# Kernel optimization log

Hardware: AMD Instinct MI355X
Metric: run time of the kernel (lower is better)

## Reference

```python
import jax, jax.numpy as jnp
import numpy as np
from jax import lax

HEADS = 8
LN_EPS = 1e-5


def setup_inputs() -> dict:
    key = jax.random.key(0)
    k = jax.random.split(key, 8)
    B, C, H, W, r = 4, 64, 64, 64, 4
    T = H * W
    x = jax.random.normal(k[0], (B, C, H, W), dtype=jnp.float32)
    conv_w = jax.random.normal(k[1], (C, C, r, r), dtype=jnp.float32) * 0.02  # OIHW
    conv_b = jnp.zeros((C,), dtype=jnp.float32)
    ln_g = jnp.ones((C,), dtype=jnp.float32)
    ln_b = jnp.zeros((C,), dtype=jnp.float32)
    Wqkv = jax.random.normal(k[2], (C, 3 * C), dtype=jnp.float32) * 0.02  # to_qvk (no bias)
    W0 = jax.random.normal(k[3], (C, C), dtype=jnp.float32) * 0.02  # output proj (no bias)
    E = jax.random.normal(k[4], (T, T // 4), dtype=jnp.float32)  # Linformer proj (randn in torch fwd)
    return {"x": x, "conv_w": conv_w, "conv_b": conv_b, "ln_g": ln_g,
            "ln_b": ln_b, "Wqkv": Wqkv, "W0": W0, "E": E}


def _layernorm2d(y, g, b):
    # LayerNorm over channel dim of NCHW (torch: permute to NHWC, LN last dim)
    yt = y.transpose(0, 2, 3, 1)  # b h w c
    mu = yt.mean(-1, keepdims=True)
    var = ((yt - mu) ** 2).mean(-1, keepdims=True)
    yt = (yt - mu) * lax.rsqrt(var + LN_EPS) * g + b
    return yt.transpose(0, 3, 1, 2)


def reference(x, conv_w, conv_b, ln_g, ln_b, Wqkv, W0, E):
    B, C, H, W = x.shape
    T = H * W
    dh = C // HEADS
    r = conv_w.shape[-1]

    # reducer: conv(stride=r) + LayerNorm2d. NOTE: faithful to the torch module,
    # this result is computed but NEVER used by the output (dead code in source).
    red = lax.conv_general_dilated(x, conv_w, (r, r), 'VALID',
                                   dimension_numbers=('NCHW', 'OIHW', 'NCHW'))
    red = red + conv_b[None, :, None, None]
    _red = _layernorm2d(red, ln_g, ln_b)  # unused, matches source

    # tokens from full-resolution x: b c h w -> b (h w) c
    xf = x.reshape(B, C, T).transpose(0, 2, 1)  # [B,T,C]
    qkv = xf @ Wqkv  # [B,T,3C]
    # rearrange 'b t (d k h)' with k=3, h=HEADS -> composite order (d, k, h)
    qkv = qkv.reshape(B, T, dh, 3, HEADS)
    q = qkv[:, :, :, 0, :].transpose(0, 3, 1, 2)  # [B,h,T,d]
    kk = qkv[:, :, :, 1, :].transpose(0, 3, 1, 2)
    v = qkv[:, :, :, 2, :].transpose(0, 3, 1, 2)

    # Linformer low-rank projection of V and K: [B,h,T,d] x [T,k] -> [B,h,k,d]
    v = jnp.einsum('bhjd,jk->bhkd', v, E)
    kk = jnp.einsum('bhjd,jk->bhkd', kk, E)

    scale = dh ** -0.5
    scores = jnp.einsum('bhid,bhjd->bhij', q, kk) * scale  # [B,h,T,k]
    attn = jax.nn.softmax(scores, axis=-1)
    out = jnp.einsum('bhij,bhjd->bhid', attn, v)  # [B,h,T,d]

    out = out.transpose(0, 2, 1, 3).reshape(B, T, C)  # b h i d -> b i (h d)
    out = out @ W0  # [B,T,C]
    return out.transpose(0, 2, 1).reshape(B, C, H, W)
```

## Files before the change

### kernel.cpp

```cpp
#include <hip/hip_runtime.h>

#define T_DIM 4096
#define KD    1024
#define SCALE 0.35355339059327373f

typedef __attribute__((ext_vector_type(8))) short bf16x8;
typedef __attribute__((ext_vector_type(4))) short bf16x4;
typedef __attribute__((ext_vector_type(4))) float f32x4;

__device__ inline unsigned short f2bf(float f) {
  unsigned u = __float_as_uint(f);
  unsigned r = u + 0x7fffu + ((u >> 16) & 1u);
  return (unsigned short)(r >> 16);
}

__device__ inline unsigned cvt_pk_bf16(float a, float b) {
  unsigned ua = __float_as_uint(a); ua += 0x7fffu + ((ua >> 16) & 1u);
  unsigned ub = __float_as_uint(b); ub += 0x7fffu + ((ub >> 16) & 1u);
  return (ua >> 16) | (ub & 0xffff0000u);
}

__device__ inline unsigned pk_trunc(float a, float b) {
  return (__float_as_uint(a) >> 16) | (__float_as_uint(b) & 0xffff0000u);
}

__device__ inline bf16x4 mk4(unsigned lo, unsigned hi) {
  union { unsigned u[2]; bf16x4 v; } x; x.u[0] = lo; x.u[1] = hi; return x.v;
}

__device__ inline bf16x8 mk8(unsigned a, unsigned b, unsigned c, unsigned d) {
  union { unsigned u[4]; bf16x8 v; } x;
  x.u[0] = a; x.u[1] = b; x.u[2] = c; x.u[3] = d; return x.v;
}

__device__ inline f32x4 mfma16(bf16x4 a, bf16x4 b, f32x4 c) {
  bf16x8 a8 = {}, b8 = {};
  a8[0] = a[0]; a8[1] = a[1]; a8[2] = a[2]; a8[3] = a[3];
  b8[0] = b[0]; b8[1] = b[1]; b8[2] = b[2]; b8[3] = b[3];
  return __builtin_amdgcn_mfma_f32_16x16x32_bf16(a8, b8, c, 0, 0, 0);
}

__global__ __launch_bounds__(256) void k_front(const float* __restrict__ x,
                                               const float* __restrict__ E,
                                               const float* __restrict__ Wqkv,
                                               float* __restrict__ partial,
                                               float* __restrict__ Q,
                                               float* __restrict__ out) {
  const int bid = blockIdx.x;
  const int tid = threadIdx.x;

  ((float4*)out)[(size_t)bid * 256 + tid] = make_float4(0.f, 0.f, 0.f, 0.f);

  if (bid < 512) {
    const int kb = bid & 7;
    const int b  = (bid >> 3) & 3;
    const int s  = bid >> 5;
    const int k0 = kb * 128;
    const int lane = tid & 63;
    const int w = tid >> 6;
    const int li = lane & 15, lg = lane >> 4;

    f32x4 acc[4][2] = {};
#pragma unroll 2
    for (int tb = 0; tb < 8; ++tb) {
      const int tbase = s * 256 + tb * 32 + lg * 8;
      bf16x8 bq[2];
#pragma unroll
      for (int nt = 0; nt < 2; ++nt) {
        const int kcol = k0 + w * 32 + nt * 16 + li;
        float bv[8];
#pragma unroll
        for (int j = 0; j < 8; ++j)
          bv[j] = E[(size_t)(tbase + j) * KD + kcol];
        bq[nt] = mk8(cvt_pk_bf16(bv[0], bv[1]), cvt_pk_bf16(bv[2], bv[3]),
                     cvt_pk_bf16(bv[4], bv[5]), cvt_pk_bf16(bv[6], bv[7]));
      }
#pragma unroll
      for (int mt = 0; mt < 4; ++mt) {
        const float* ap = x + ((size_t)b * 64 + mt * 16 + li) * T_DIM + tbase;
        float4 a0 = *(const float4*)(ap);
        float4 a1 = *(const float4*)(ap + 4);
        bf16x8 af8 = mk8(cvt_pk_bf16(a0.x, a0.y), cvt_pk_bf16(a0.z, a0.w),
                         cvt_pk_bf16(a1.x, a1.y), cvt_pk_bf16(a1.z, a1.w));
        acc[mt][0] = __builtin_amdgcn_mfma_f32_16x16x32_bf16(af8, bq[0], acc[mt][0], 0, 0, 0);
        acc[mt][1] = __builtin_amdgcn_mfma_f32_16x16x32_bf16(af8, bq[1], acc[mt][1], 0, 0, 0);
      }
    }
    float* pb = partial + ((size_t)s * 4 + b) * (64 * KD);
#pragma unroll
    for (int mt = 0; mt < 4; ++mt)
#pragma unroll
      for (int nt = 0; nt < 2; ++nt) {
        const int row = mt * 16 + lg * 4;
        const int col = k0 + w * 32 + nt * 16 + li;
#pragma unroll
        for (int reg = 0; reg < 4; ++reg)
          pb[(size_t)(row + reg) * KD + col] = acc[mt][nt][reg];
      }
  } else {
    const int idx = bid - 512;
    const int g  = idx & 7;
    const int tt = (idx >> 3) & 15;
    const int b  = idx >> 7;
    const int t  = tt * 256 + tid;
    const int col0 = g * 24;

    float acc[8];
#pragma unroll
    for (int j = 0; j < 8; ++j) acc[j] = 0.f;
    const float* xb = x + (size_t)b * 64 * T_DIM + t;
#pragma unroll 4
    for (int c = 0; c < 64; ++c) {
      float xv = xb[(size_t)c * T_DIM];
      const float* wr = Wqkv + c * 192 + col0;
#pragma unroll
      for (int h = 0; h < 8; ++h) acc[h] += xv * wr[h];
    }
#pragma unroll
    for (int h = 0; h < 8; ++h)
      Q[(((size_t)(b * 8 + h)) * 8 + g) * T_DIM + t] = acc[h];
  }
}

__global__ __launch_bounds__(256) void k_xkv(const float* __restrict__ partial,
                                             const float* __restrict__ Wqkv,
                                             uint2* __restrict__ Kg,
                                             unsigned short* __restrict__ Vg) {
  __shared__ unsigned short XPs[64 * 72];
  const int kb = blockIdx.x;
  const int h  = blockIdx.y;
  const int b  = blockIdx.z;
  const int tid = threadIdx.x;

  {
    const int kk = tid & 63;
    const int cg = tid >> 6;
#pragma unroll
    for (int u = 0; u < 16; ++u) {
      const int c = cg * 16 + u;
      const size_t src = (size_t)c * KD + kb * 64 + kk;
      float a = 0.f;
#pragma unroll
      for (int s = 0; s < 16; ++s)
        a += partial[((size_t)s * 4 + b) * (64 * KD) + src];
      XPs[c * 72 + kk] = f2bf(a);
    }
  }
  __syncthreads();

  const int klocal = tid & 63;
  const int sel    = (tid >> 6) & 1;
  const int dg     = tid >> 7;
  const int k      = kb * 64 + klocal;

  float acc[4];
#pragma unroll
  for (int d = 0; d < 4; ++d) acc[d] = 0.f;
#pragma unroll 4
  for (int c = 0; c < 64; ++c) {
    float xv = __uint_as_float((unsigned)XPs[c * 72 + klocal] << 16);
    const float* wr = Wqkv + c * 192 + (sel + 1) * 8 + h;
#pragma unroll
    for (int d = 0; d < 4; ++d) acc[d] += xv * wr[(dg * 4 + d) * 24];
  }

  const int bh = b * 8 + h;
  if (sel == 0) {
    uint2* kg = Kg + (size_t)bh * 2048;
    kg[dg * 1024 + k] = make_uint2(cvt_pk_bf16(acc[0] * SCALE, acc[1] * SCALE),
                                   cvt_pk_bf16(acc[2] * SCALE, acc[3] * SCALE));
  } else {
#pragma unroll
    for (int d = 0; d < 4; ++d)
      Vg[(size_t)(bh * 8 + dg * 4 + d) * KD + k] = f2bf(acc[d]);
  }
}

#define VT_PITCH 1032
__global__ __launch_bounds__(256) void k_attn(const float* __restrict__ Q,
                                              const uint2* __restrict__ Kg,
                                              const unsigned short* __restrict__ Vg,
                                              const float* __restrict__ W0,
                                              float* __restrict__ out) {
  __shared__ __attribute__((aligned(16))) unsigned short Kt[2 * 1024 * 4];
  __shared__ unsigned short Vt[9 * VT_PITCH];
  __shared__ float W0s[512];
  const int bh = blockIdx.x;
  const int tid = threadIdx.x;
  const int b = bh >> 3, h = bh & 7;

  const uint2* kg = Kg + (size_t)bh * 2048;
  uint2* kt2 = (uint2*)Kt;
#pragma unroll
  for (int it = 0; it < 8; ++it)
    kt2[it * 256 + tid] = kg[it * 256 + tid];
  const unsigned* vg = (const unsigned*)(Vg + (size_t)bh * 8192);
#pragma unroll
  for (int dd = 0; dd < 8; ++dd) {
#pragma unroll
    for (int it = 0; it < 2; ++it) {
      const int j2 = it * 256 + tid;
      *(unsigned*)(Vt + dd * VT_PITCH + j2 * 2) = vg[dd * 512 + j2];
    }
  }
#pragma unroll
  for (int it = 0; it < 2; ++it)
    *(unsigned*)(Vt + 8 * VT_PITCH + (it * 256 + tid) * 2) = 0x3F803F80u;
  W0s[tid]       = W0[h * 512 + tid];
  W0s[tid + 256] = W0[h * 512 + tid + 256];
  __syncthreads();

  const int lane = tid & 63, w = tid >> 6;
  const int li = lane & 15, lg = lane >> 4;
  const int i0w = blockIdx.y * 128 + w * 32;

  bf16x4 qf[2] = {bf16x4{}, bf16x4{}};
  if (lane < 32) {
#pragma unroll
    for (int it2 = 0; it2 < 2; ++it2) {
      const float* qp = Q + ((size_t)bh * 8 + lg * 4) * T_DIM + i0w + it2 * 16 + li;
      qf[it2] = mk4(cvt_pk_bf16(qp[0], qp[T_DIM]),
                    cvt_pk_bf16(qp[2 * T_DIM], qp[3 * T_DIM]));
    }
  }

  f32x4 accO[2] = {f32x4{0.f, 0.f, 0.f, 0.f}, f32x4{0.f, 0.f, 0.f, 0.f}};
#pragma unroll 2
  for (int jt = 0; jt < 1024; jt += 16) {
    bf16x4 kf = {};
    if (lane < 32) kf = *(const bf16x4*)(&Kt[(size_t)(lg * 1024 + jt + li) * 4]);
    bf16x4 vf = {};
    if (li < 9) vf = *(const bf16x4*)(&Vt[li * VT_PITCH + jt + lg * 4]);
#pragma unroll
    for (int it2 = 0; it2 < 2; ++it2) {
      f32x4 st = mfma16(kf, qf[it2], f32x4{0.f, 0.f, 0.f, 0.f});
      f32x4 p;
      p[0] = __expf(st[0]); p[1] = __expf(st[1]);
      p[2] = __expf(st[2]); p[3] = __expf(st[3]);
      bf16x4 pf = mk4(pk_trunc(p[0], p[1]), pk_trunc(p[2], p[3]));
      accO[it2] = mfma16(vf, pf, accO[it2]);
    }
  }

  __syncthreads();
  float* OwW = (float*)Kt + w * 256;

#pragma unroll
  for (int it2 = 0; it2 < 2; ++it2) {
    float l = __shfl(accO[it2][0], 32 + li);
    float inv = 1.0f / l;
    if (lane < 32) {
      float4 o = make_float4(accO[it2][0] * inv, accO[it2][1] * inv,
                             accO[it2][2] * inv, accO[it2][3] * inv);
      *(float4*)(OwW + (it2 * 16 + li) * 8 + lg * 4) = o;
    }
  }

  const int tok = lane & 31, ch = lane >> 5;
  float ov[8];
#pragma unroll
  for (int d = 0; d < 8; ++d) ov[d] = OwW[tok * 8 + d];
#pragma unroll 4
  for (int j = 0; j < 32; ++j) {
    const int c = ch * 32 + j;
    float a = 0.f;
#pragma unroll
    for (int d = 0; d < 8; ++d) a += ov[d] * W0s[d * 64 + c];
    atomicAdd(out + ((size_t)b * 64 + c) * T_DIM + i0w + tok, a);
  }
}

extern "C" void kernel_launch(void* const* d_in, const int* in_sizes, int n_in,
                              void* d_out, int out_size, void* d_ws, size_t ws_size,
                              hipStream_t stream) {
  const float* x    = (const float*)d_in[0];
  const float* Wqkv = (const float*)d_in[5];
  const float* W0   = (const float*)d_in[6];
  const float* E    = (const float*)d_in[7];
  float* out = (float*)d_out;

  float* Q           = (float*)d_ws;
  float* partial     = Q + 1048576;
  uint2* Kg          = (uint2*)(partial + 4194304);
  unsigned short* Vg = (unsigned short*)(Kg + 65536);

  k_front <<<dim3(1024),     256, 0, stream>>>(x, E, Wqkv, partial, Q, out);
  k_xkv   <<<dim3(16, 8, 4), 256, 0, stream>>>(partial, Wqkv, Kg, Vg);
  k_attn  <<<dim3(32, 32),   256, 0, stream>>>(Q, Kg, Vg, W0, out);
}
```

Baseline: 149.3 us.

## Split-K reduction into separate kernel and fold log2e into K scale for exp2

Previously every (kb,h,b) block of k_xkv re-summed the 16 split-K partials, so each head block repeated the same reduction, eight times over. A new k_red kernel sums them once with float4 loads into an fp32 buffer, and k_xkv reads that buffer directly. The attention softmax now uses native exp2, with log2(e) folded into the K scale so the hardware exp2 instruction can be used. This adds one kernel launch and an extra global round trip for the reduced buffer, and the exponent now comes from a native approximation.

```diff
diff --git a/kernel.cpp b/kernel.cpp
--- a/kernel.cpp
+++ b/kernel.cpp
@@ -3,6 +3,9 @@
 #define T_DIM 4096
 #define KD    1024
 #define SCALE 0.35355339059327373f
+#define SCALE2 (0.35355339059327373f * 1.4426950408889634f)
+
+extern "C" __device__ float __ocml_native_exp2_f32(float);
 
 typedef __attribute__((ext_vector_type(8))) short bf16x8;
 typedef __attribute__((ext_vector_type(4))) short bf16x4;
@@ -122,43 +125,42 @@
   }
 }
 
-__global__ __launch_bounds__(256) void k_xkv(const float* __restrict__ partial,
+__global__ __launch_bounds__(256) void k_red(const float* __restrict__ partial,
+                                             float* __restrict__ XPf) {
+  const int gid = blockIdx.x * 256 + threadIdx.x;
+  const int b  = gid >> 14;
+  const int ck = gid & 16383;
+  const float4* p4 = (const float4*)partial;
+  float4 a = make_float4(0.f, 0.f, 0.f, 0.f);
+#pragma unroll
+  for (int s = 0; s < 16; ++s) {
+    float4 v = p4[(size_t)(s * 4 + b) * 16384 + ck];
+    a.x += v.x; a.y += v.y; a.z += v.z; a.w += v.w;
+  }
+  ((float4*)XPf)[gid] = a;
+}
+
+__global__ __launch_bounds__(256) void k_xkv(const float* __restrict__ XPf,
                                              const float* __restrict__ Wqkv,
                                              uint2* __restrict__ Kg,
                                              unsigned short* __restrict__ Vg) {
-  __shared__ unsigned short XPs[64 * 72];
   const int kb = blockIdx.x;
   const int h  = blockIdx.y;
   const int b  = blockIdx.z;
   const int tid = threadIdx.x;
 
-  {
-    const int kk = tid & 63;
-    const int cg = tid >> 6;
-#pragma unroll
-    for (int u = 0; u < 16; ++u) {
-      const int c = cg * 16 + u;
-      const size_t src = (size_t)c * KD + kb * 64 + kk;
-      float a = 0.f;
-#pragma unroll
-      for (int s = 0; s < 16; ++s)
-        a += partial[((size_t)s * 4 + b) * (64 * KD) + src];
-      XPs[c * 72 + kk] = f2bf(a);
-    }
-  }
-  __syncthreads();
-
   const int klocal = tid & 63;
   const int sel    = (tid >> 6) & 1;
   const int dg     = tid >> 7;
   const int k      = kb * 64 + klocal;
 
+  const float* xp = XPf + (size_t)b * 65536 + k;
   float acc[4];
 #pragma unroll
   for (int d = 0; d < 4; ++d) acc[d] = 0.f;
-#pragma unroll 4
+#pragma unroll 8
   for (int c = 0; c < 64; ++c) {
-    float xv = __uint_as_float((unsigned)XPs[c * 72 + klocal] << 16);
+    float xv = xp[(size_t)c * KD];
     const float* wr = Wqkv + c * 192 + (sel + 1) * 8 + h;
 #pragma unroll
     for (int d = 0; d < 4; ++d) acc[d] += xv * wr[(dg * 4 + d) * 24];
@@ -167,8 +169,8 @@
   const int bh = b * 8 + h;
   if (sel == 0) {
     uint2* kg = Kg + (size_t)bh * 2048;
-    kg[dg * 1024 + k] = make_uint2(cvt_pk_bf16(acc[0] * SCALE, acc[1] * SCALE),
-                                   cvt_pk_bf16(acc[2] * SCALE, acc[3] * SCALE));
+    kg[dg * 1024 + k] = make_uint2(cvt_pk_bf16(acc[0] * SCALE2, acc[1] * SCALE2),
+                                   cvt_pk_bf16(acc[2] * SCALE2, acc[3] * SCALE2));
   } else {
 #pragma unroll
     for (int d = 0; d < 4; ++d)
@@ -235,8 +237,8 @@
     for (int it2 = 0; it2 < 2; ++it2) {
       f32x4 st = mfma16(kf, qf[it2], f32x4{0.f, 0.f, 0.f, 0.f});
       f32x4 p;
-      p[0] = __expf(st[0]); p[1] = __expf(st[1]);
-      p[2] = __expf(st[2]); p[3] = __expf(st[3]);
+      p[0] = __ocml_native_exp2_f32(st[0]); p[1] = __ocml_native_exp2_f32(st[1]);
+      p[2] = __ocml_native_exp2_f32(st[2]); p[3] = __ocml_native_exp2_f32(st[3]);
       bf16x4 pf = mk4(pk_trunc(p[0], p[1]), pk_trunc(p[2], p[3]));
       accO[it2] = mfma16(vf, pf, accO[it2]);
     }
@@ -283,8 +285,10 @@
   float* partial     = Q + 1048576;
   uint2* Kg          = (uint2*)(partial + 4194304);
   unsigned short* Vg = (unsigned short*)(Kg + 65536);
+  float* XPf         = (float*)(Vg + 262144);
 
   k_front <<<dim3(1024),     256, 0, stream>>>(x, E, Wqkv, partial, Q, out);
-  k_xkv   <<<dim3(16, 8, 4), 256, 0, stream>>>(partial, Wqkv, Kg, Vg);
+  k_red   <<<dim3(256),      256, 0, stream>>>(partial, XPf);
+  k_xkv   <<<dim3(16, 8, 4), 256, 0, stream>>>(XPf, Wqkv, Kg, Vg);
   k_attn  <<<dim3(32, 32),   256, 0, stream>>>(Q, Kg, Vg, W0, out);
 }
```

New measurement: 149.0 us. Within noise of the previous version (-0.2%).

## Halve split-K partials, double attention tokens per block, fold log2e into K scale

Applied to the files above, without the earlier changes.

The front kernel now uses 8 split-T slices of 512 tokens instead of 16 of 256, which halves the partial buffer and the reduction reads in k_xkv. k_xkv keeps the reduced X·E in fp32 shared memory instead of bf16. k_attn processes two token tiles per block so the K/V shared-memory staging is amortised over twice the work, with half as many blocks. Softmax uses native exp2 with log2e folded into the K scale. The trade-offs are fewer blocks in flight for the front and attention kernels, and the larger per-block zeroing of the output now spread over 512 blocks.

```diff
diff --git a/kernel.cpp b/kernel.cpp
--- a/kernel.cpp
+++ b/kernel.cpp
@@ -3,6 +3,10 @@
 #define T_DIM 4096
 #define KD    1024
 #define SCALE 0.35355339059327373f
+#define SCALE2 (0.35355339059327373f * 1.4426950408889634f)
+#define VT_PITCH 1032
+
+extern "C" __device__ float __ocml_native_exp2_f32(float);
 
 typedef __attribute__((ext_vector_type(8))) short bf16x8;
 typedef __attribute__((ext_vector_type(4))) short bf16x4;
@@ -49,9 +53,13 @@
   const int bid = blockIdx.x;
   const int tid = threadIdx.x;
 
-  ((float4*)out)[(size_t)bid * 256 + tid] = make_float4(0.f, 0.f, 0.f, 0.f);
-
   if (bid < 512) {
+    float4* o4 = (float4*)out;
+    o4[(size_t)bid * 512 + tid]       = make_float4(0.f, 0.f, 0.f, 0.f);
+    o4[(size_t)bid * 512 + tid + 256] = make_float4(0.f, 0.f, 0.f, 0.f);
+  }
+
+  if (bid < 256) {
     const int kb = bid & 7;
     const int b  = (bid >> 3) & 3;
     const int s  = bid >> 5;
@@ -62,8 +70,8 @@
 
     f32x4 acc[4][2] = {};
 #pragma unroll 2
-    for (int tb = 0; tb < 8; ++tb) {
-      const int tbase = s * 256 + tb * 32 + lg * 8;
+    for (int tb = 0; tb < 16; ++tb) {
+      const int tbase = s * 512 + tb * 32 + lg * 8;
       bf16x8 bq[2];
 #pragma unroll
       for (int nt = 0; nt < 2; ++nt) {
@@ -98,7 +106,7 @@
           pb[(size_t)(row + reg) * KD + col] = acc[mt][nt][reg];
       }
   } else {
-    const int idx = bid - 512;
+    const int idx = bid - 256;
     const int g  = idx & 7;
     const int tt = (idx >> 3) & 15;
     const int b  = idx >> 7;
@@ -126,7 +134,7 @@
                                              const float* __restrict__ Wqkv,
                                              uint2* __restrict__ Kg,
                                              unsigned short* __restrict__ Vg) {
-  __shared__ unsigned short XPs[64 * 72];
+  __shared__ float XPs[64 * 64];
   const int kb = blockIdx.x;
   const int h  = blockIdx.y;
   const int b  = blockIdx.z;
@@ -135,15 +143,15 @@
   {
     const int kk = tid & 63;
     const int cg = tid >> 6;
-#pragma unroll
+#pragma unroll 4
     for (int u = 0; u < 16; ++u) {
       const int c = cg * 16 + u;
       const size_t src = (size_t)c * KD + kb * 64 + kk;
       float a = 0.f;
 #pragma unroll
-      for (int s = 0; s < 16; ++s)
+      for (int s = 0; s < 8; ++s)
         a += partial[((size_t)s * 4 + b) * (64 * KD) + src];
-      XPs[c * 72 + kk] = f2bf(a);
+      XPs[c * 64 + kk] = a;
     }
   }
   __syncthreads();
@@ -156,9 +164,9 @@
   float acc[4];
 #pragma unroll
   for (int d = 0; d < 4; ++d) acc[d] = 0.f;
-#pragma unroll 4
+#pragma unroll 8
   for (int c = 0; c < 64; ++c) {
-    float xv = __uint_as_float((unsigned)XPs[c * 72 + klocal] << 16);
+    float xv = XPs[c * 64 + klocal];
     const float* wr = Wqkv + c * 192 + (sel + 1) * 8 + h;
 #pragma unroll
     for (int d = 0; d < 4; ++d) acc[d] += xv * wr[(dg * 4 + d) * 24];
@@ -167,8 +175,8 @@
   const int bh = b * 8 + h;
   if (sel == 0) {
     uint2* kg = Kg + (size_t)bh * 2048;
-    kg[dg * 1024 + k] = make_uint2(cvt_pk_bf16(acc[0] * SCALE, acc[1] * SCALE),
-                                   cvt_pk_bf16(acc[2] * SCALE, acc[3] * SCALE));
+    kg[dg * 1024 + k] = make_uint2(cvt_pk_bf16(acc[0] * SCALE2, acc[1] * SCALE2),
+                                   cvt_pk_bf16(acc[2] * SCALE2, acc[3] * SCALE2));
   } else {
 #pragma unroll
     for (int d = 0; d < 4; ++d)
@@ -176,7 +184,6 @@
   }
 }
 
-#define VT_PITCH 1032
 __global__ __launch_bounds__(256) void k_attn(const float* __restrict__ Q,
                                               const uint2* __restrict__ Kg,
                                               const unsigned short* __restrict__ Vg,
@@ -186,6 +193,7 @@
   __shared__ unsigned short Vt[9 * VT_PITCH];
   __shared__ float W0s[512];
   const int bh = blockIdx.x;
+  const int iy = blockIdx.y;
   const int tid = threadIdx.x;
   const int b = bh >> 3, h = bh & 7;
 
@@ -212,19 +220,24 @@
 
   const int lane = tid & 63, w = tid >> 6;
   const int li = lane & 15, lg = lane >> 4;
-  const int i0w = blockIdx.y * 128 + w * 32;
-
-  bf16x4 qf[2] = {bf16x4{}, bf16x4{}};
+
+  bf16x4 qf[2][2];
+#pragma unroll
+  for (int tt = 0; tt < 2; ++tt) { qf[tt][0] = bf16x4{}; qf[tt][1] = bf16x4{}; }
   if (lane < 32) {
 #pragma unroll
-    for (int it2 = 0; it2 < 2; ++it2) {
-      const float* qp = Q + ((size_t)bh * 8 + lg * 4) * T_DIM + i0w + it2 * 16 + li;
-      qf[it2] = mk4(cvt_pk_bf16(qp[0], qp[T_DIM]),
-                    cvt_pk_bf16(qp[2 * T_DIM], qp[3 * T_DIM]));
-    }
-  }
-
-  f32x4 accO[2] = {f32x4{0.f, 0.f, 0.f, 0.f}, f32x4{0.f, 0.f, 0.f, 0.f}};
+    for (int tt = 0; tt < 2; ++tt) {
+      const int i0 = (iy + tt * 16) * 128 + w * 32;
+#pragma unroll
+      for (int it2 = 0; it2 < 2; ++it2) {
+        const float* qp = Q + ((size_t)bh * 8 + lg * 4) * T_DIM + i0 + it2 * 16 + li;
+        qf[tt][it2] = mk4(cvt_pk_bf16(qp[0], qp[T_DIM]),
+                          cvt_pk_bf16(qp[2 * T_DIM], qp[3 * T_DIM]));
+      }
+    }
+  }
+
+  f32x4 accO[2][2] = {};
 #pragma unroll 2
   for (int jt = 0; jt < 1024; jt += 16) {
     bf16x4 kf = {};
@@ -232,41 +245,47 @@
     bf16x4 vf = {};
     if (li < 9) vf = *(const bf16x4*)(&Vt[li * VT_PITCH + jt + lg * 4]);
 #pragma unroll
-    for (int it2 = 0; it2 < 2; ++it2) {
-      f32x4 st = mfma16(kf, qf[it2], f32x4{0.f, 0.f, 0.f, 0.f});
-      f32x4 p;
-      p[0] = __expf(st[0]); p[1] = __expf(st[1]);
-      p[2] = __expf(st[2]); p[3] = __expf(st[3]);
-      bf16x4 pf = mk4(pk_trunc(p[0], p[1]), pk_trunc(p[2], p[3]));
-      accO[it2] = mfma16(vf, pf, accO[it2]);
-    }
+    for (int tt = 0; tt < 2; ++tt)
+#pragma unroll
+      for (int it2 = 0; it2 < 2; ++it2) {
+        f32x4 st = mfma16(kf, qf[tt][it2], f32x4{0.f, 0.f, 0.f, 0.f});
+        f32x4 p;
+        p[0] = __ocml_native_exp2_f32(st[0]); p[1] = __ocml_native_exp2_f32(st[1]);
+        p[2] = __ocml_native_exp2_f32(st[2]); p[3] = __ocml_native_exp2_f32(st[3]);
+        bf16x4 pf = mk4(pk_trunc(p[0], p[1]), pk_trunc(p[2], p[3]));
+        accO[tt][it2] = mfma16(vf, pf, accO[tt][it2]);
+      }
   }
 
   __syncthreads();
   float* OwW = (float*)Kt + w * 256;
-
-#pragma unroll
-  for (int it2 = 0; it2 < 2; ++it2) {
-    float l = __shfl(accO[it2][0], 32 + li);
-    float inv = 1.0f / l;
-    if (lane < 32) {
-      float4 o = make_float4(accO[it2][0] * inv, accO[it2][1] * inv,
-                             accO[it2][2] * inv, accO[it2][3] * inv);
-      *(float4*)(OwW + (it2 * 16 + li) * 8 + lg * 4) = o;
-    }
-  }
-
   const int tok = lane & 31, ch = lane >> 5;
-  float ov[8];
-#pragma unroll
-  for (int d = 0; d < 8; ++d) ov[d] = OwW[tok * 8 + d];
+
+#pragma unroll
+  for (int tt = 0; tt < 2; ++tt) {
+    const int i0 = (iy + tt * 16) * 128 + w * 32;
+#pragma unroll
+    for (int it2 = 0; it2 < 2; ++it2) {
+      float l = __shfl(accO[tt][it2][0], 32 + li);
+      float inv = 1.0f / l;
+      if (lane < 32) {
+        float4 o = make_float4(accO[tt][it2][0] * inv, accO[tt][it2][1] * inv,
+                               accO[tt][it2][2] * inv, accO[tt][it2][3] * inv);
+        *(float4*)(OwW + (it2 * 16 + li) * 8 + lg * 4) = o;
+      }
+    }
+
+    float ov[8];
+#pragma unroll
+    for (int d = 0; d < 8; ++d) ov[d] = OwW[tok * 8 + d];
 #pragma unroll 4
-  for (int j = 0; j < 32; ++j) {
-    const int c = ch * 32 + j;
-    float a = 0.f;
-#pragma unroll
-    for (int d = 0; d < 8; ++d) a += ov[d] * W0s[d * 64 + c];
-    atomicAdd(out + ((size_t)b * 64 + c) * T_DIM + i0w + tok, a);
+    for (int j = 0; j < 32; ++j) {
+      const int c = ch * 32 + j;
+      float a = 0.f;
+#pragma unroll
+      for (int d = 0; d < 8; ++d) a += ov[d] * W0s[d * 64 + c];
+      atomicAdd(out + ((size_t)b * 64 + c) * T_DIM + i0 + tok, a);
+    }
   }
 }
 
@@ -281,10 +300,10 @@
 
   float* Q           = (float*)d_ws;
   float* partial     = Q + 1048576;
-  uint2* Kg          = (uint2*)(partial + 4194304);
+  uint2* Kg          = (uint2*)(partial + 2097152);
   unsigned short* Vg = (unsigned short*)(Kg + 65536);
 
-  k_front <<<dim3(1024),     256, 0, stream>>>(x, E, Wqkv, partial, Q, out);
+  k_front <<<dim3(768),      256, 0, stream>>>(x, E, Wqkv, partial, Q, out);
   k_xkv   <<<dim3(16, 8, 4), 256, 0, stream>>>(partial, Wqkv, Kg, Vg);
-  k_attn  <<<dim3(32, 32),   256, 0, stream>>>(Q, Kg, Vg, W0, out);
-}
+  k_attn  <<<dim3(32, 16),   256, 0, stream>>>(Q, Kg, Vg, W0, out);
+}
```

New measurement: 159.2 us. +6.7%, slower.

## Fuse Q projection into attention, halve split-K partials, use exp2 softmax

Applied to the files above, without the earlier changes.

The Q projection moves out of the front kernel and into the attention kernel, which computes Q tiles directly from x using a per-head slice of Wqkv staged in shared memory. This removes the Q workspace round trip. The front kernel now runs 256 blocks, each covering twice the token range, so there are half as many split-K partials to write and reduce. The reduction keeps fp32 in shared memory instead of rounding to bf16. Softmax uses native exp2 with log2(e) folded into the K scale, while x is read again inside each attention block and the front grid becomes smaller.

```diff
diff --git a/kernel.cpp b/kernel.cpp
--- a/kernel.cpp
+++ b/kernel.cpp
@@ -3,6 +3,10 @@
 #define T_DIM 4096
 #define KD    1024
 #define SCALE 0.35355339059327373f
+#define SCALE2 (0.35355339059327373f * 1.4426950408889634f)
+#define VT_PITCH 1032
+
+extern "C" __device__ float __ocml_native_exp2_f32(float);
 
 typedef __attribute__((ext_vector_type(8))) short bf16x8;
 typedef __attribute__((ext_vector_type(4))) short bf16x4;
@@ -42,91 +46,70 @@
 
 __global__ __launch_bounds__(256) void k_front(const float* __restrict__ x,
                                                const float* __restrict__ E,
-                                               const float* __restrict__ Wqkv,
                                                float* __restrict__ partial,
-                                               float* __restrict__ Q,
                                                float* __restrict__ out) {
   const int bid = blockIdx.x;
   const int tid = threadIdx.x;
 
-  ((float4*)out)[(size_t)bid * 256 + tid] = make_float4(0.f, 0.f, 0.f, 0.f);
-
-  if (bid < 512) {
-    const int kb = bid & 7;
-    const int b  = (bid >> 3) & 3;
-    const int s  = bid >> 5;
-    const int k0 = kb * 128;
-    const int lane = tid & 63;
-    const int w = tid >> 6;
-    const int li = lane & 15, lg = lane >> 4;
-
-    f32x4 acc[4][2] = {};
+  {
+    float4* o4 = (float4*)out;
+#pragma unroll
+    for (int u = 0; u < 4; ++u)
+      o4[(size_t)bid * 1024 + u * 256 + tid] = make_float4(0.f, 0.f, 0.f, 0.f);
+  }
+
+  const int kb = bid & 7;
+  const int b  = (bid >> 3) & 3;
+  const int s  = bid >> 5;
+  const int k0 = kb * 128;
+  const int lane = tid & 63;
+  const int w = tid >> 6;
+  const int li = lane & 15, lg = lane >> 4;
+
+  f32x4 acc[4][2] = {};
 #pragma unroll 2
-    for (int tb = 0; tb < 8; ++tb) {
-      const int tbase = s * 256 + tb * 32 + lg * 8;
-      bf16x8 bq[2];
-#pragma unroll
-      for (int nt = 0; nt < 2; ++nt) {
-        const int kcol = k0 + w * 32 + nt * 16 + li;
-        float bv[8];
-#pragma unroll
-        for (int j = 0; j < 8; ++j)
-          bv[j] = E[(size_t)(tbase + j) * KD + kcol];
-        bq[nt] = mk8(cvt_pk_bf16(bv[0], bv[1]), cvt_pk_bf16(bv[2], bv[3]),
-                     cvt_pk_bf16(bv[4], bv[5]), cvt_pk_bf16(bv[6], bv[7]));
-      }
-#pragma unroll
-      for (int mt = 0; mt < 4; ++mt) {
-        const float* ap = x + ((size_t)b * 64 + mt * 16 + li) * T_DIM + tbase;
-        float4 a0 = *(const float4*)(ap);
-        float4 a1 = *(const float4*)(ap + 4);
-        bf16x8 af8 = mk8(cvt_pk_bf16(a0.x, a0.y), cvt_pk_bf16(a0.z, a0.w),
-                         cvt_pk_bf16(a1.x, a1.y), cvt_pk_bf16(a1.z, a1.w));
-        acc[mt][0] = __builtin_amdgcn_mfma_f32_16x16x32_bf16(af8, bq[0], acc[mt][0], 0, 0, 0);
-        acc[mt][1] = __builtin_amdgcn_mfma_f32_16x16x32_bf16(af8, bq[1], acc[mt][1], 0, 0, 0);
-      }
-    }
-    float* pb = partial + ((size_t)s * 4 + b) * (64 * KD);
-#pragma unroll
-    for (int mt = 0; mt < 4; ++mt)
-#pragma unroll
-      for (int nt = 0; nt < 2; ++nt) {
-        const int row = mt * 16 + lg * 4;
-        const int col = k0 + w * 32 + nt * 16 + li;
-#pragma unroll
-        for (int reg = 0; reg < 4; ++reg)
-          pb[(size_t)(row + reg) * KD + col] = acc[mt][nt][reg];
-      }
-  } else {
-    const int idx = bid - 512;
-    const int g  = idx & 7;
-    const int tt = (idx >> 3) & 15;
-    const int b  = idx >> 7;
-    const int t  = tt * 256 + tid;
-    const int col0 = g * 24;
-
-    float acc[8];
-#pragma unroll
-    for (int j = 0; j < 8; ++j) acc[j] = 0.f;
-    const float* xb = x + (size_t)b * 64 * T_DIM + t;
-#pragma unroll 4
-    for (int c = 0; c < 64; ++c) {
-      float xv = xb[(size_t)c * T_DIM];
-      const float* wr = Wqkv + c * 192 + col0;
-#pragma unroll
-      for (int h = 0; h < 8; ++h) acc[h] += xv * wr[h];
-    }
-#pragma unroll
-    for (int h = 0; h < 8; ++h)
-      Q[(((size_t)(b * 8 + h)) * 8 + g) * T_DIM + t] = acc[h];
-  }
+  for (int tb = 0; tb < 16; ++tb) {
+    const int tbase = s * 512 + tb * 32 + lg * 8;
+    bf16x8 bq[2];
+#pragma unroll
+    for (int nt = 0; nt < 2; ++nt) {
+      const int kcol = k0 + w * 32 + nt * 16 + li;
+      float bv[8];
+#pragma unroll
+      for (int j = 0; j < 8; ++j)
+        bv[j] = E[(size_t)(tbase + j) * KD + kcol];
+      bq[nt] = mk8(cvt_pk_bf16(bv[0], bv[1]), cvt_pk_bf16(bv[2], bv[3]),
+                   cvt_pk_bf16(bv[4], bv[5]), cvt_pk_bf16(bv[6], bv[7]));
+    }
+#pragma unroll
+    for (int mt = 0; mt < 4; ++mt) {
+      const float* ap = x + ((size_t)b * 64 + mt * 16 + li) * T_DIM + tbase;
+      float4 a0 = *(const float4*)(ap);
+      float4 a1 = *(const float4*)(ap + 4);
+      bf16x8 af8 = mk8(cvt_pk_bf16(a0.x, a0.y), cvt_pk_bf16(a0.z, a0.w),
+                       cvt_pk_bf16(a1.x, a1.y), cvt_pk_bf16(a1.z, a1.w));
+      acc[mt][0] = __builtin_amdgcn_mfma_f32_16x16x32_bf16(af8, bq[0], acc[mt][0], 0, 0, 0);
+      acc[mt][1] = __builtin_amdgcn_mfma_f32_16x16x32_bf16(af8, bq[1], acc[mt][1], 0, 0, 0);
+    }
+  }
+  float* pb = partial + ((size_t)s * 4 + b) * (64 * KD);
+#pragma unroll
+  for (int mt = 0; mt < 4; ++mt)
+#pragma unroll
+    for (int nt = 0; nt < 2; ++nt) {
+      const int row = mt * 16 + lg * 4;
+      const int col = k0 + w * 32 + nt * 16 + li;
+#pragma unroll
+      for (int reg = 0; reg < 4; ++reg)
+        pb[(size_t)(row + reg) * KD + col] = acc[mt][nt][reg];
+    }
 }
 
 __global__ __launch_bounds__(256) void k_xkv(const float* __restrict__ partial,
                                              const float* __restrict__ Wqkv,
                                              uint2* __restrict__ Kg,
                                              unsigned short* __restrict__ Vg) {
-  __shared__ unsigned short XPs[64 * 72];
+  __shared__ float XPs[64 * 64];
   const int kb = blockIdx.x;
   const int h  = blockIdx.y;
   const int b  = blockIdx.z;
@@ -135,15 +118,15 @@
   {
     const int kk = tid & 63;
     const int cg = tid >> 6;
-#pragma unroll
+#pragma unroll 4
     for (int u = 0; u < 16; ++u) {
       const int c = cg * 16 + u;
       const size_t src = (size_t)c * KD + kb * 64 + kk;
       float a = 0.f;
 #pragma unroll
-      for (int s = 0; s < 16; ++s)
+      for (int s = 0; s < 8; ++s)
         a += partial[((size_t)s * 4 + b) * (64 * KD) + src];
-      XPs[c * 72 + kk] = f2bf(a);
+      XPs[c * 64 + kk] = a;
     }
   }
   __syncthreads();
@@ -156,9 +139,9 @@
   float acc[4];
 #pragma unroll
   for (int d = 0; d < 4; ++d) acc[d] = 0.f;
-#pragma unroll 4
+#pragma unroll 8
   for (int c = 0; c < 64; ++c) {
-    float xv = __uint_as_float((unsigned)XPs[c * 72 + klocal] << 16);
+    float xv = XPs[c * 64 + klocal];
     const float* wr = Wqkv + c * 192 + (sel + 1) * 8 + h;
 #pragma unroll
     for (int d = 0; d < 4; ++d) acc[d] += xv * wr[(dg * 4 + d) * 24];
@@ -167,8 +150,8 @@
   const int bh = b * 8 + h;
   if (sel == 0) {
     uint2* kg = Kg + (size_t)bh * 2048;
-    kg[dg * 1024 + k] = make_uint2(cvt_pk_bf16(acc[0] * SCALE, acc[1] * SCALE),
-                                   cvt_pk_bf16(acc[2] * SCALE, acc[3] * SCALE));
+    kg[dg * 1024 + k] = make_uint2(cvt_pk_bf16(acc[0] * SCALE2, acc[1] * SCALE2),
+                                   cvt_pk_bf16(acc[2] * SCALE2, acc[3] * SCALE2));
   } else {
 #pragma unroll
     for (int d = 0; d < 4; ++d)
@@ -176,8 +159,8 @@
   }
 }
 
-#define VT_PITCH 1032
-__global__ __launch_bounds__(256) void k_attn(const float* __restrict__ Q,
+__global__ __launch_bounds__(256) void k_attn(const float* __restrict__ x,
+                                              const float* __restrict__ Wqkv,
                                               const uint2* __restrict__ Kg,
                                               const unsigned short* __restrict__ Vg,
                                               const float* __restrict__ W0,
@@ -185,6 +168,7 @@
   __shared__ __attribute__((aligned(16))) unsigned short Kt[2 * 1024 * 4];
   __shared__ unsigned short Vt[9 * VT_PITCH];
   __shared__ float W0s[512];
+  __shared__ float Wqh[512];
   const int bh = blockIdx.x;
   const int tid = threadIdx.x;
   const int b = bh >> 3, h = bh & 7;
@@ -208,6 +192,11 @@
     *(unsigned*)(Vt + 8 * VT_PITCH + (it * 256 + tid) * 2) = 0x3F803F80u;
   W0s[tid]       = W0[h * 512 + tid];
   W0s[tid + 256] = W0[h * 512 + tid + 256];
+#pragma unroll
+  for (int e = tid; e < 512; e += 256) {
+    const int c = e >> 3, d = e & 7;
+    Wqh[e] = Wqkv[c * 192 + d * 24 + h];
+  }
   __syncthreads();
 
   const int lane = tid & 63, w = tid >> 6;
@@ -216,12 +205,20 @@
 
   bf16x4 qf[2] = {bf16x4{}, bf16x4{}};
   if (lane < 32) {
-#pragma unroll
-    for (int it2 = 0; it2 < 2; ++it2) {
-      const float* qp = Q + ((size_t)bh * 8 + lg * 4) * T_DIM + i0w + it2 * 16 + li;
-      qf[it2] = mk4(cvt_pk_bf16(qp[0], qp[T_DIM]),
-                    cvt_pk_bf16(qp[2 * T_DIM], qp[3 * T_DIM]));
-    }
+    float qa0[4] = {0.f, 0.f, 0.f, 0.f}, qa1[4] = {0.f, 0.f, 0.f, 0.f};
+    const float* xb = x + (size_t)b * 64 * T_DIM + i0w + li;
+#pragma unroll 4
+    for (int c = 0; c < 64; ++c) {
+      const float4 wq = *(const float4*)(&Wqh[c * 8 + lg * 4]);
+      const float xv0 = xb[(size_t)c * T_DIM];
+      const float xv1 = xb[(size_t)c * T_DIM + 16];
+      qa0[0] += xv0 * wq.x; qa0[1] += xv0 * wq.y;
+      qa0[2] += xv0 * wq.z; qa0[3] += xv0 * wq.w;
+      qa1[0] += xv1 * wq.x; qa1[1] += xv1 * wq.y;
+      qa1[2] += xv1 * wq.z; qa1[3] += xv1 * wq.w;
+    }
+    qf[0] = mk4(cvt_pk_bf16(qa0[0], qa0[1]), cvt_pk_bf16(qa0[2], qa0[3]));
+    qf[1] = mk4(cvt_pk_bf16(qa1[0], qa1[1]), cvt_pk_bf16(qa1[2], qa1[3]));
   }
 
   f32x4 accO[2] = {f32x4{0.f, 0.f, 0.f, 0.f}, f32x4{0.f, 0.f, 0.f, 0.f}};
@@ -235,8 +232,8 @@
     for (int it2 = 0; it2 < 2; ++it2) {
       f32x4 st = mfma16(kf, qf[it2], f32x4{0.f, 0.f, 0.f, 0.f});
       f32x4 p;
-      p[0] = __expf(st[0]); p[1] = __expf(st[1]);
-      p[2] = __expf(st[2]); p[3] = __expf(st[3]);
+      p[0] = __ocml_native_exp2_f32(st[0]); p[1] = __ocml_native_exp2_f32(st[1]);
+      p[2] = __ocml_native_exp2_f32(st[2]); p[3] = __ocml_native_exp2_f32(st[3]);
       bf16x4 pf = mk4(pk_trunc(p[0], p[1]), pk_trunc(p[2], p[3]));
       accO[it2] = mfma16(vf, pf, accO[it2]);
     }
@@ -279,12 +276,11 @@
   const float* E    = (const float*)d_in[7];
   float* out = (float*)d_out;
 
-  float* Q           = (float*)d_ws;
-  float* partial     = Q + 1048576;
-  uint2* Kg          = (uint2*)(partial + 4194304);
+  float* partial     = (float*)d_ws;
+  uint2* Kg          = (uint2*)(partial + 2097152);
   unsigned short* Vg = (unsigned short*)(Kg + 65536);
 
-  k_front <<<dim3(1024),     256, 0, stream>>>(x, E, Wqkv, partial, Q, out);
+  k_front <<<dim3(256),      256, 0, stream>>>(x, E, partial, out);
   k_xkv   <<<dim3(16, 8, 4), 256, 0, stream>>>(partial, Wqkv, Kg, Vg);
-  k_attn  <<<dim3(32, 32),   256, 0, stream>>>(Q, Kg, Vg, W0, out);
-}
+  k_attn  <<<dim3(32, 32),   256, 0, stream>>>(x, Wqkv, Kg, Vg, W0, out);
+}
```

Result: slower. 162.5 us (+8.9%).
